# Optimization experiments

Measured on AMD Instinct MI355X. Metric: run time of the kernel, lower is better.

## Reference

```python
import jax, jax.numpy as jnp
import numpy as np

B, N, D, H = 8, 1024, 768, 12
HD = D // H
SCALE = HD ** -0.5

def setup_inputs() -> dict:
    key = jax.random.key(0)
    k1, k2, k3, k4 = jax.random.split(key, 4)
    x = jax.random.normal(k1, (B, N, D), dtype=jnp.float32)
    weight = jax.random.uniform(k2, (B, N), dtype=jnp.float32)
    W_qkv = jax.random.normal(k3, (D, 3 * D), dtype=jnp.float32) * (D ** -0.5)
    W_msa = jax.random.normal(k4, (D, D), dtype=jnp.float32) * (D ** -0.5)
    b_msa = jnp.zeros((D,), dtype=jnp.float32)
    return {"x": x, "weight": weight, "W_qkv": W_qkv, "W_msa": W_msa, "b_msa": b_msa}

def reference(x, weight, W_qkv, W_msa, b_msa):
    # QKV projection (no bias), then elementwise per-token gate
    qkv = jnp.einsum('bnd,de->bne', x, W_qkv)          # [B,N,3D]
    qkv = weight[:, :, None] * qkv
    qkv = qkv.reshape(B, N, 3, H, HD).transpose(2, 0, 3, 1, 4)  # [3,B,H,N,hd]
    q, k, v = qkv[0], qkv[1], qkv[2]
    A = jnp.einsum('bhnd,bhmd->bhnm', q, k) * SCALE    # [B,H,N,N]
    A = jax.nn.softmax(A, axis=-1)
    out = jnp.einsum('bhnm,bhmd->bhnd', A, v)          # [B,H,N,hd]
    out = out.transpose(0, 2, 1, 3).reshape(B, N, D)
    return jnp.einsum('bnd,de->bne', out, W_msa) + b_msa
```

## Files before the change

kernel.cpp:

```cpp
#include <hip/hip_runtime.h>
#include <hip/hip_bf16.h>


typedef __attribute__((ext_vector_type(8))) short bf8;
typedef __attribute__((ext_vector_type(4))) float f4;

#define QSCALE 0.1803368801111204f

static __device__ __forceinline__ short bf16_of(float f) {
    union { float f; unsigned u; } a; a.f = f;
    unsigned r = a.u + 0x7FFFu + ((a.u >> 16) & 1u);
    return (short)(r >> 16);
}

static __device__ __forceinline__ unsigned bfpk(float lo, float hi) {
    float2 t; t.x = lo; t.y = hi;
    __hip_bfloat162 b = __float22bfloat162_rn(t);
    union { __hip_bfloat162 b; unsigned u; } c; c.b = b;
    return c.u;
}

static __device__ __forceinline__ void async16(const short* g, short* l) {
    __builtin_amdgcn_global_load_lds(
        (const __attribute__((address_space(1))) void*)g,
        (__attribute__((address_space(3))) void*)l, 16, 0, 0);
}

__global__ __launch_bounds__(256) void k_cvt(const float* __restrict__ src,
                                             const float* __restrict__ gate,
                                             short* __restrict__ dst, int n8) {
    int i = blockIdx.x * 256 + threadIdx.x;
    if (i >= n8) return;
    const float g = gate[i / 96];
    const f4* sp = (const f4*)src;
    f4 a = sp[2 * i], b = sp[2 * i + 1];
    union { bf8 v; short h[8]; } o;
    o.h[0] = bf16_of(a[0] * g); o.h[1] = bf16_of(a[1] * g);
    o.h[2] = bf16_of(a[2] * g); o.h[3] = bf16_of(a[3] * g);
    o.h[4] = bf16_of(b[0] * g); o.h[5] = bf16_of(b[1] * g);
    o.h[6] = bf16_of(b[2] * g); o.h[7] = bf16_of(b[3] * g);
    ((bf8*)dst)[i] = o.v;
}

__global__ __launch_bounds__(256) void k_transpose(const float* __restrict__ w,
                                                   short* __restrict__ wt,
                                                   int K, int E) {
    __shared__ short t[64][65];
    const int k0 = blockIdx.y * 64, e0 = blockIdx.x * 64;
    const int tid = threadIdx.x;
#pragma unroll
    for (int p = 0; p < 16; ++p) {
        int idx = p * 256 + tid;
        int r = idx >> 6, c = idx & 63;
        t[r][c] = bf16_of(w[(k0 + r) * E + e0 + c]);
    }
    __syncthreads();
#pragma unroll
    for (int p = 0; p < 16; ++p) {
        int idx = p * 256 + tid;
        int r = idx >> 6, c = idx & 63;
        wt[(e0 + r) * K + k0 + c] = t[c][r];
    }
}

static __device__ __forceinline__ void gemm128(const short* __restrict__ gA,
                                               const short* __restrict__ gB,
                                               short* smem,
                                               f4 acc[4][4]) {
    const int tid = threadIdx.x, lane = tid & 63;
    const int l16 = lane & 15, quad = lane >> 4, rx = l16 & 7;
    const int wm = (tid >> 6) & 1, wn = tid >> 7;

    auto stage = [&](short* S, int k0) {
#pragma unroll
        for (int c = 0; c < 4; ++c) {
            int p = c * 256 + tid;
            int row = p >> 3, slot = p & 7;
            int gc = slot ^ (row & 7);
            async16(gA + row * 768 + k0 + gc * 8, S + p * 8);
            async16(gB + row * 768 + k0 + gc * 8, S + 8192 + p * 8);
        }
    };

    stage(smem, 0);
    for (int it = 0; it < 12; ++it) {
        __builtin_amdgcn_s_waitcnt(0);
        __syncthreads();
        short* Sc = smem + (it & 1) * 16384;
        if (it + 1 < 12) stage(smem + ((it + 1) & 1) * 16384, (it + 1) * 64);
        const short* As = Sc;
        const short* Bs = Sc + 8192;
#pragma unroll
        for (int ks = 0; ks < 2; ++ks) {
            bf8 af[4], bfr[4];
#pragma unroll
            for (int mt = 0; mt < 4; ++mt)
                af[mt] = *(const bf8*)(As + (wm * 64 + mt * 16 + l16) * 64 +
                                       (((ks * 4 + quad) ^ rx) * 8));
#pragma unroll
            for (int nt = 0; nt < 4; ++nt)
                bfr[nt] = *(const bf8*)(Bs + (wn * 64 + nt * 16 + l16) * 64 +
                                        (((ks * 4 + quad) ^ rx) * 8));
#pragma unroll
            for (int mt = 0; mt < 4; ++mt)
#pragma unroll
                for (int nt = 0; nt < 4; ++nt)
                    acc[mt][nt] = __builtin_amdgcn_mfma_f32_16x16x32_bf16(
                        af[mt], bfr[nt], acc[mt][nt], 0, 0, 0);
        }
    }
    __syncthreads();
}

__global__ __launch_bounds__(256) void k_gemm_qkv(
        const short* __restrict__ xb, const short* __restrict__ wtq,
        short* __restrict__ qb, short* __restrict__ kb, short* __restrict__ vt) {
    __shared__ short smem[32768];
    const int tid = threadIdx.x, lane = tid & 63;
    const int l16 = lane & 15, quad = lane >> 4;
    const int wm = (tid >> 6) & 1, wn = tid >> 7;
    const int m0 = blockIdx.y * 128, n0 = blockIdx.x * 128;
    f4 z = {0.f, 0.f, 0.f, 0.f};
    f4 acc[4][4] = {{z,z,z,z},{z,z,z,z},{z,z,z,z},{z,z,z,z}};
    gemm128(xb + m0 * 768, wtq + n0 * 768, smem, acc);

    const int which = n0 / 768;
    if (which < 2) {
#pragma unroll
        for (int mt = 0; mt < 4; ++mt) {
#pragma unroll
            for (int r = 0; r < 4; ++r) {
                const int row = m0 + wm * 64 + mt * 16 + quad * 4 + r;
                const int b = row >> 10, nn = row & 1023;
#pragma unroll
                for (int nt = 0; nt < 4; ++nt) {
                    const int ct = n0 + wn * 64 + nt * 16;
                    const int h = (ct - which * 768) >> 6;
                    const int hh = b * 12 + h;
                    const int hd = (ct & 63) + l16;
                    const float val = acc[mt][nt][r];
                    if (which == 0)
                        qb[(hh * 1024 + nn) * 64 + hd] = bf16_of(val * QSCALE);
                    else
                        kb[(hh * 1024 + nn) * 64 + hd] = bf16_of(val);
                }
            }
        }
    } else {
#pragma unroll
        for (int mt = 0; mt < 4; ++mt) {
#pragma unroll
            for (int r = 0; r < 4; ++r) {
                const int tok = wm * 64 + mt * 16 + quad * 4 + r;
#pragma unroll
                for (int nt = 0; nt < 4; ++nt) {
                    const int dim = wn * 64 + nt * 16 + l16;
                    smem[dim * 132 + tok] = bf16_of(acc[mt][nt][r]);
                }
            }
        }
        __syncthreads();
        const int b = m0 >> 10, nn0 = m0 & 1023;
#pragma unroll
        for (int ps = 0; ps < 8; ++ps) {
            const int row = ps * 16 + (tid >> 4);
            const int chunk = tid & 15;
            const int dg = (n0 - 1536) + row;
            const int h = dg >> 6, hd = dg & 63;
            bf8 val = *(const bf8*)(smem + row * 132 + chunk * 8);
            *(bf8*)(vt + ((b * 12 + h) * 64 + hd) * 1024 + nn0 + chunk * 8) = val;
        }
    }
}

__global__ __launch_bounds__(256) void k_gemm_final(
        const short* __restrict__ attn, const short* __restrict__ wtm,
        const float* __restrict__ bias, float* __restrict__ out) {
    __shared__ short smem[32768];
    const int lane = threadIdx.x & 63;
    const int l16 = lane & 15, quad = lane >> 4;
    const int wm = (threadIdx.x >> 6) & 1, wn = threadIdx.x >> 7;
    const int m0 = blockIdx.y * 128, n0 = blockIdx.x * 128;
    f4 z = {0.f, 0.f, 0.f, 0.f};
    f4 acc[4][4] = {{z,z,z,z},{z,z,z,z},{z,z,z,z},{z,z,z,z}};
    gemm128(attn + m0 * 768, wtm + n0 * 768, smem, acc);
#pragma unroll
    for (int mt = 0; mt < 4; ++mt) {
#pragma unroll
        for (int r = 0; r < 4; ++r) {
            const int row = m0 + wm * 64 + mt * 16 + quad * 4 + r;
#pragma unroll
            for (int nt = 0; nt < 4; ++nt) {
                const int e = n0 + wn * 64 + nt * 16 + l16;
                out[row * 768 + e] = acc[mt][nt][r] + bias[e];
            }
        }
    }
}

__global__ __launch_bounds__(512) void k_attn(const short* __restrict__ qb,
                                              const short* __restrict__ kb,
                                              const short* __restrict__ vt,
                                              short* __restrict__ attn) {
    __shared__ short Ks[2][4096];
    __shared__ short Vs[2][4096];
    const int tid = threadIdx.x, wave = tid >> 6, lane = tid & 63;
    const int l16 = lane & 15, quad = lane >> 4;
    const int bh = blockIdx.x;
    const int b = bh / 12, h = bh - b * 12;
    const int m_base = blockIdx.y * 128 + wave * 16;
    const short* qh = qb + bh * 65536;
    const short* kh = kb + bh * 65536;
    const short* vh = vt + bh * 65536;

    const int rA = ((l16 >> 2) << 3) + (l16 & 3);
    const int fK = (((rA >> 3) & 1) << 2) + (rA & 3);
    const int sK = (quad ^ fK) * 8;
    const int oAlo = rA * 64 + sK;
    const int oAhi = rA * 64 + (sK ^ 32);
    const int oBlo = oAlo + 256, oBhi = oAhi + 256;
    const int fV = (((l16 >> 3) & 1) << 2) + (l16 & 3);
    const int oV = l16 * 64 + ((quad ^ fV) * 8);

    const short* qp = qh + (m_base + l16) * 64 + quad * 8;
    bf8 qf0 = *(const bf8*)(qp);
    bf8 qf1 = *(const bf8*)(qp + 32);

    union { bf8 v; short h[8]; } onef;
#pragma unroll
    for (int i = 0; i < 8; ++i) onef.h[i] = (short)0x3F80;

    f4 z = {0.f, 0.f, 0.f, 0.f};
    f4 acc[4] = {z, z, z, z};
    f4 accl = z;

    auto stage = [&](int buf, int j0) {
        int idx = tid;
        int row = idx >> 3;
        int fr = (((row >> 3) & 1) << 2) + (row & 3);
        int gc = (idx & 7) ^ fr;
        async16(kh + (j0 + row) * 64 + gc * 8, Ks[buf] + idx * 8);
        async16(vh + row * 1024 + j0 + gc * 8, Vs[buf] + idx * 8);
    };

    stage(0, 0);
    int cur = 0;
    for (int it = 0; it < 16; ++it) {
        __builtin_amdgcn_s_waitcnt(0);
        __syncthreads();
        if (it + 1 < 16) stage(cur ^ 1, (it + 1) * 64);
        const short* Kc = Ks[cur];
        const short* Vc = Vs[cur];

#pragma unroll
        for (int jj = 0; jj < 64; jj += 32) {
            const short* kjj = Kc + jj * 64;
            bf8 kAlo = *(const bf8*)(kjj + oAlo);
            bf8 kAhi = *(const bf8*)(kjj + oAhi);
            bf8 kBlo = *(const bf8*)(kjj + oBlo);
            bf8 kBhi = *(const bf8*)(kjj + oBhi);

            f4 sA = z, sB = z;
            sA = __builtin_amdgcn_mfma_f32_16x16x32_bf16(kAlo, qf0, sA, 0, 0, 0);
            sA = __builtin_amdgcn_mfma_f32_16x16x32_bf16(kAhi, qf1, sA, 0, 0, 0);
            sB = __builtin_amdgcn_mfma_f32_16x16x32_bf16(kBlo, qf0, sB, 0, 0, 0);
            sB = __builtin_amdgcn_mfma_f32_16x16x32_bf16(kBhi, qf1, sB, 0, 0, 0);
            float a0 = __builtin_amdgcn_exp2f(sA[0]);
            float a1 = __builtin_amdgcn_exp2f(sA[1]);
            float a2 = __builtin_amdgcn_exp2f(sA[2]);
            float a3 = __builtin_amdgcn_exp2f(sA[3]);
            float b0 = __builtin_amdgcn_exp2f(sB[0]);
            float b1 = __builtin_amdgcn_exp2f(sB[1]);
            float b2 = __builtin_amdgcn_exp2f(sB[2]);
            float b3 = __builtin_amdgcn_exp2f(sB[3]);
            union { bf8 v; unsigned u[4]; } p;
            p.u[0] = bfpk(a0, a1); p.u[1] = bfpk(a2, a3);
            p.u[2] = bfpk(b0, b1); p.u[3] = bfpk(b2, b3);
            accl = __builtin_amdgcn_mfma_f32_16x16x32_bf16(
                onef.v, p.v, accl, 0, 0, 0);

#pragma unroll
            for (int dt = 0; dt < 4; ++dt) {
                bf8 vf = *(const bf8*)(Vc + dt * 1024 + (oV ^ (jj ? 32 : 0)));
                acc[dt] = __builtin_amdgcn_mfma_f32_16x16x32_bf16(
                    vf, p.v, acc[dt], 0, 0, 0);
            }
        }
        cur ^= 1;
    }

    const float inv = 1.f / accl[0];
    const int row = (b << 10) + m_base + l16;
    short* op = attn + row * 768 + h * 64 + quad * 4;
#pragma unroll
    for (int dt = 0; dt < 4; ++dt)
#pragma unroll
        for (int r = 0; r < 4; ++r)
            op[dt * 16 + r] = bf16_of(acc[dt][r] * inv);
}

extern "C" void kernel_launch(void* const* d_in, const int* in_sizes, int n_in,
                              void* d_out, int out_size, void* d_ws, size_t ws_size,
                              hipStream_t stream) {
    const float* x    = (const float*)d_in[0];
    const float* gate = (const float*)d_in[1];
    const float* Wqkv = (const float*)d_in[2];
    const float* Wmsa = (const float*)d_in[3];
    const float* bmsa = (const float*)d_in[4];
    float* out = (float*)d_out;

    char* ws = (char*)d_ws;
    short* xb  = (short*)(ws);
    short* wtq = (short*)(ws + 12582912);
    short* wtm = (short*)(ws + 16121856);
    short* qb  = (short*)(ws + 17301504);
    short* kb  = (short*)(ws + 29884416);
    short* vt  = (short*)(ws + 42467328);
    short* attn = xb;

    k_cvt<<<3072, 256, 0, stream>>>(x, gate, xb, 786432);
    k_transpose<<<dim3(36, 12), 256, 0, stream>>>(Wqkv, wtq, 768, 2304);
    k_transpose<<<dim3(12, 12), 256, 0, stream>>>(Wmsa, wtm, 768, 768);
    k_gemm_qkv<<<dim3(18, 64), 256, 0, stream>>>(xb, wtq, qb, kb, vt);
    k_attn<<<dim3(96, 8), 512, 0, stream>>>(qb, kb, vt, attn);
    k_gemm_final<<<dim3(6, 64), 256, 0, stream>>>(attn, wtm, bmsa, out);
}
```

Baseline: 186.1 us.

## Merge prep kernels into one launch and shrink GEMM K-tile to 32

Combines the activation conversion kernel and the two weight-transpose kernels into a single k_prep launch, which removes two kernel launches and their gaps. The shared GEMM routine moves from a 64-wide K tile to a 32-wide K tile. Each tile pairs two rows into a 64-element LDS line with a new XOR swizzle, and shared memory per block is halved. This is meant to raise occupancy and cut LDS bank conflicts. The cost is twice as many barriers and sync points over 24 iterations, with less MFMA work between each.

```diff
diff --git a/kernel.cpp b/kernel.cpp
--- a/kernel.cpp
+++ b/kernel.cpp
@@ -26,28 +26,31 @@
         (__attribute__((address_space(3))) void*)l, 16, 0, 0);
 }
 
-__global__ __launch_bounds__(256) void k_cvt(const float* __restrict__ src,
-                                             const float* __restrict__ gate,
-                                             short* __restrict__ dst, int n8) {
-    int i = blockIdx.x * 256 + threadIdx.x;
-    if (i >= n8) return;
-    const float g = gate[i / 96];
-    const f4* sp = (const f4*)src;
-    f4 a = sp[2 * i], b = sp[2 * i + 1];
-    union { bf8 v; short h[8]; } o;
-    o.h[0] = bf16_of(a[0] * g); o.h[1] = bf16_of(a[1] * g);
-    o.h[2] = bf16_of(a[2] * g); o.h[3] = bf16_of(a[3] * g);
-    o.h[4] = bf16_of(b[0] * g); o.h[5] = bf16_of(b[1] * g);
-    o.h[6] = bf16_of(b[2] * g); o.h[7] = bf16_of(b[3] * g);
-    ((bf8*)dst)[i] = o.v;
-}
-
-__global__ __launch_bounds__(256) void k_transpose(const float* __restrict__ w,
-                                                   short* __restrict__ wt,
-                                                   int K, int E) {
+__global__ __launch_bounds__(256) void k_prep(
+        const float* __restrict__ x, const float* __restrict__ gate,
+        short* __restrict__ xb,
+        const float* __restrict__ Wqkv, short* __restrict__ wtq,
+        const float* __restrict__ Wmsa, short* __restrict__ wtm) {
     __shared__ short t[64][65];
-    const int k0 = blockIdx.y * 64, e0 = blockIdx.x * 64;
-    const int tid = threadIdx.x;
+    const int bx = blockIdx.x, tid = threadIdx.x;
+    if (bx < 3072) {
+        int i = bx * 256 + tid;
+        const float g = gate[i / 96];
+        const f4* sp = (const f4*)x;
+        f4 a = sp[2 * i], b = sp[2 * i + 1];
+        union { bf8 v; short h[8]; } o;
+        o.h[0] = bf16_of(a[0] * g); o.h[1] = bf16_of(a[1] * g);
+        o.h[2] = bf16_of(a[2] * g); o.h[3] = bf16_of(a[3] * g);
+        o.h[4] = bf16_of(b[0] * g); o.h[5] = bf16_of(b[1] * g);
+        o.h[6] = bf16_of(b[2] * g); o.h[7] = bf16_of(b[3] * g);
+        ((bf8*)xb)[i] = o.v;
+        return;
+    }
+    const float* w; short* wt; int E, f;
+    if (bx < 3504) { w = Wqkv; wt = wtq; E = 2304; f = bx - 3072; }
+    else           { w = Wmsa; wt = wtm; E = 768;  f = bx - 3504; }
+    const int et = (E == 2304) ? 36 : 12;
+    const int e0 = (f % et) * 64, k0 = (f / et) * 64;
 #pragma unroll
     for (int p = 0; p < 16; ++p) {
         int idx = p * 256 + tid;
@@ -59,7 +62,7 @@
     for (int p = 0; p < 16; ++p) {
         int idx = p * 256 + tid;
         int r = idx >> 6, c = idx & 63;
-        wt[(e0 + r) * K + k0 + c] = t[c][r];
+        wt[(e0 + r) * 768 + k0 + c] = t[c][r];
     }
 }
 
@@ -68,46 +71,44 @@
                                                short* smem,
                                                f4 acc[4][4]) {
     const int tid = threadIdx.x, lane = tid & 63;
-    const int l16 = lane & 15, quad = lane >> 4, rx = l16 & 7;
+    const int l16 = lane & 15, quad = lane >> 4;
     const int wm = (tid >> 6) & 1, wn = tid >> 7;
 
     auto stage = [&](short* S, int k0) {
 #pragma unroll
-        for (int c = 0; c < 4; ++c) {
-            int p = c * 256 + tid;
-            int row = p >> 3, slot = p & 7;
-            int gc = slot ^ (row & 7);
-            async16(gA + row * 768 + k0 + gc * 8, S + p * 8);
-            async16(gB + row * 768 + k0 + gc * 8, S + 8192 + p * 8);
+        for (int i = 0; i < 2; ++i) {
+            int p = i * 256 + tid;
+            int L = p >> 3, sl = p & 7;
+            int r = 2 * L + (sl >> 2);
+            int c = (sl & 3) ^ (L & 3);
+            async16(gA + r * 768 + k0 + c * 8, S + p * 8);
+            async16(gB + r * 768 + k0 + c * 8, S + 4096 + p * 8);
         }
     };
+    const int sq = (l16 >> 1) & 3;
+    const int aoff = (l16 >> 1) * 64 + (l16 & 1) * 32 + ((quad ^ sq) * 8);
 
     stage(smem, 0);
-    for (int it = 0; it < 12; ++it) {
+    for (int it = 0; it < 24; ++it) {
         __builtin_amdgcn_s_waitcnt(0);
         __syncthreads();
-        short* Sc = smem + (it & 1) * 16384;
-        if (it + 1 < 12) stage(smem + ((it + 1) & 1) * 16384, (it + 1) * 64);
-        const short* As = Sc;
-        const short* Bs = Sc + 8192;
-#pragma unroll
-        for (int ks = 0; ks < 2; ++ks) {
-            bf8 af[4], bfr[4];
-#pragma unroll
-            for (int mt = 0; mt < 4; ++mt)
-                af[mt] = *(const bf8*)(As + (wm * 64 + mt * 16 + l16) * 64 +
-                                       (((ks * 4 + quad) ^ rx) * 8));
+        short* Sc = smem + (it & 1) * 8192;
+        if (it + 1 < 24) stage(smem + ((it + 1) & 1) * 8192, (it + 1) * 32);
+        const short* As = Sc + wm * 2048;
+        const short* Bs = Sc + 4096 + wn * 2048;
+        bf8 af[4], bfr[4];
+#pragma unroll
+        for (int mt = 0; mt < 4; ++mt)
+            af[mt] = *(const bf8*)(As + mt * 512 + aoff);
+#pragma unroll
+        for (int nt = 0; nt < 4; ++nt)
+            bfr[nt] = *(const bf8*)(Bs + nt * 512 + aoff);
+#pragma unroll
+        for (int mt = 0; mt < 4; ++mt)
 #pragma unroll
             for (int nt = 0; nt < 4; ++nt)
-                bfr[nt] = *(const bf8*)(Bs + (wn * 64 + nt * 16 + l16) * 64 +
-                                        (((ks * 4 + quad) ^ rx) * 8));
-#pragma unroll
-            for (int mt = 0; mt < 4; ++mt)
-#pragma unroll
-                for (int nt = 0; nt < 4; ++nt)
-                    acc[mt][nt] = __builtin_amdgcn_mfma_f32_16x16x32_bf16(
-                        af[mt], bfr[nt], acc[mt][nt], 0, 0, 0);
-        }
+                acc[mt][nt] = __builtin_amdgcn_mfma_f32_16x16x32_bf16(
+                    af[mt], bfr[nt], acc[mt][nt], 0, 0, 0);
     }
     __syncthreads();
 }
@@ -115,7 +116,7 @@
 __global__ __launch_bounds__(256) void k_gemm_qkv(
         const short* __restrict__ xb, const short* __restrict__ wtq,
         short* __restrict__ qb, short* __restrict__ kb, short* __restrict__ vt) {
-    __shared__ short smem[32768];
+    __shared__ short smem[16896];
     const int tid = threadIdx.x, lane = tid & 63;
     const int l16 = lane & 15, quad = lane >> 4;
     const int wm = (tid >> 6) & 1, wn = tid >> 7;
@@ -176,7 +177,7 @@
 __global__ __launch_bounds__(256) void k_gemm_final(
         const short* __restrict__ attn, const short* __restrict__ wtm,
         const float* __restrict__ bias, float* __restrict__ out) {
-    __shared__ short smem[32768];
+    __shared__ short smem[16384];
     const int lane = threadIdx.x & 63;
     const int l16 = lane & 15, quad = lane >> 4;
     const int wm = (threadIdx.x >> 6) & 1, wn = threadIdx.x >> 7;
@@ -318,9 +319,7 @@
     short* vt  = (short*)(ws + 42467328);
     short* attn = xb;
 
-    k_cvt<<<3072, 256, 0, stream>>>(x, gate, xb, 786432);
-    k_transpose<<<dim3(36, 12), 256, 0, stream>>>(Wqkv, wtq, 768, 2304);
-    k_transpose<<<dim3(12, 12), 256, 0, stream>>>(Wmsa, wtm, 768, 768);
+    k_prep<<<3648, 256, 0, stream>>>(x, gate, xb, Wqkv, wtq, Wmsa, wtm);
     k_gemm_qkv<<<dim3(18, 64), 256, 0, stream>>>(xb, wtq, qb, kb, vt);
     k_attn<<<dim3(96, 8), 512, 0, stream>>>(qb, kb, vt, attn);
     k_gemm_final<<<dim3(6, 64), 256, 0, stream>>>(attn, wtm, bmsa, out);
```

Result: slower. 190.7 us (+2.5%).
